# Kernel optimization log

Hardware: AMD Instinct MI355X
Metric: run time of the kernel (lower is better)

Reference implementation:

```python
import jax, jax.numpy as jnp
import numpy as np


def _maxpool2(x):
    # 2x2 max pool, stride 2, on NCHW
    b, c, h, w = x.shape
    return x.reshape(b, c, h // 2, 2, w // 2, 2).max(axis=(3, 5))


def _conv1x1(w, x):
    # w: [out_c, in_c], x: [B, in_c, H, W]
    return jnp.einsum('oc,bchw->bohw', w, x)


def setup_inputs() -> dict:
    key = jax.random.key(0)
    ks = jax.random.split(key, 5)
    B, C, H, W = 16, 64, 64, 64
    x = jax.random.normal(ks[0], (B, C, H, W), dtype=jnp.float32)
    # 1x1 conv weights (spectral-norm treated as already-normalized params)
    Wt = jax.random.normal(ks[1], (C // 8, C), dtype=jnp.float32) * 0.05
    Wp = jax.random.normal(ks[2], (C // 8, C), dtype=jnp.float32) * 0.05
    Wg = jax.random.normal(ks[3], (C // 2, C), dtype=jnp.float32) * 0.05
    Wo = jax.random.normal(ks[4], (C, C // 2), dtype=jnp.float32) * 0.05
    gamma = jnp.float32(0.5)  # nonzero so attention branch contributes
    return {"x": x, "Wt": Wt, "Wp": Wp, "Wg": Wg, "Wo": Wo, "gamma": gamma}


def reference(x, Wt, Wp, Wg, Wo, gamma):
    b, c, h, w = x.shape
    theta = _conv1x1(Wt, x).reshape(b, c // 8, h * w)            # [B, C/8, HW]
    phi = _maxpool2(_conv1x1(Wp, x)).reshape(b, c // 8, -1)      # [B, C/8, HW/4]
    g = _maxpool2(_conv1x1(Wg, x)).reshape(b, c // 2, -1)        # [B, C/2, HW/4]
    # scores: [B, HW, HW/4]; softmax over pooled (key) axis
    beta = jax.nn.softmax(jnp.einsum('bct,bcs->bts', theta, phi), axis=-1)
    o = jnp.einsum('bcs,bts->bct', g, beta).reshape(b, c // 2, h, w)
    o = _conv1x1(Wo, o)                                          # [B, C, H, W]
    return gamma * o + x
```

## Files before the change

### kernel.cpp

```cpp
#include <hip/hip_runtime.h>
#include <math.h>

#define NB   16
#define NC   64
#define HWs  4096
#define NPS  1024
#define LOG2E 1.44269504088896341f

static constexpr size_t PHI_OFF = (size_t)NB * HWs * 8;
static constexpr size_t GT_OFF  = PHI_OFF + (size_t)NB * NPS * 8;

typedef short s16x8 __attribute__((ext_vector_type(8)));
typedef float f32x4 __attribute__((ext_vector_type(4)));

#define LD8G(p) (*(const s16x8*)(p))
#define SB()    __builtin_amdgcn_sched_barrier(0)

__device__ inline unsigned short f2bf(float f) {
    unsigned int u = __float_as_uint(f);
    u += 0x7fffu + ((u >> 16) & 1u);
    return (unsigned short)(u >> 16);
}
__device__ inline unsigned int pk2(float a, float b) {
    unsigned int ua = __float_as_uint(a); ua += 0x7fffu + ((ua >> 16) & 1u);
    unsigned int ub = __float_as_uint(b); ub += 0x7fffu + ((ub >> 16) & 1u);
    return (ua >> 16) | (ub & 0xffff0000u);
}

__global__ __launch_bounds__(256) __attribute__((amdgpu_waves_per_eu(4, 4)))
void k_proj(
    const float* __restrict__ x, const float* __restrict__ Wt,
    const float* __restrict__ Wp, const float* __restrict__ Wg,
    unsigned short* __restrict__ ws)
{
    __shared__ float xs[64 * 128];

    unsigned short* theta = ws;
    unsigned short* phi   = ws + PHI_OFF;
    unsigned short* gT    = ws + GT_OFF;

    const int tid  = threadIdx.x;
    const int blk  = blockIdx.x;
    const int b    = blk >> 6;
    const int rp   = (blk >> 1) & 31;
    const int half = blk & 1;

    const float* xsrc = x + (size_t)b * NC * HWs + rp * 128;
#pragma unroll
    for (int i = 0; i < 8; ++i) {
        const int idx = i * 256 + tid;
        const int ci  = idx >> 5;
        const int f4  = idx & 31;
        float4 v = *(const float4*)(xsrc + (size_t)ci * HWs + f4 * 4);
        *(float4*)(xs + ci * 128 + f4 * 4) = v;
    }
    __syncthreads();

    const int h   = tid & 127;
    const int sub = __builtin_amdgcn_readfirstlane(tid >> 7);
    const int row = h & 1;
    const int col = h >> 1;
    const int px  = row * 64 + col;

    float a4[4], ag8[8];
#pragma unroll
    for (int j = 0; j < 4; ++j) a4[j] = 0.f;
#pragma unroll
    for (int j = 0; j < 8; ++j) ag8[j] = 0.f;

    const float* W8 = (half ? Wp : Wt) + sub * 4 * NC;
    const float* WG = Wg + (half * 16 + sub * 8) * NC;

#pragma unroll 4
    for (int ci = 0; ci < NC; ++ci) {
        const float xv = xs[ci * 128 + px];
#pragma unroll
        for (int j = 0; j < 4; ++j) a4[j] += W8[j * NC + ci] * xv;
#pragma unroll
        for (int j = 0; j < 8; ++j) ag8[j] += WG[j * NC + ci] * xv;
    }

    if (half == 0) {
        const int q = (2 * rp + row) * 64 + col;
        uint2 pkd;
        pkd.x = pk2(a4[0] * LOG2E, a4[1] * LOG2E);
        pkd.y = pk2(a4[2] * LOG2E, a4[3] * LOG2E);
        *(uint2*)(theta + ((size_t)b * HWs + q) * 8 + sub * 4) = pkd;
    } else {
#pragma unroll
        for (int j = 0; j < 4; ++j) {
            float v = a4[j];
            v = fmaxf(v, __shfl_xor(v, 1));
            v = fmaxf(v, __shfl_xor(v, 2));
            a4[j] = v;
        }
    }

#pragma unroll
    for (int j = 0; j < 8; ++j) {
        float v = ag8[j];
        v = fmaxf(v, __shfl_xor(v, 1));
        v = fmaxf(v, __shfl_xor(v, 2));
        ag8[j] = v;
    }

    if ((h & 3) == 0) {
        const int ps = rp * 32 + (h >> 2);
        if (half == 1) {
            uint2 pkd;
            pkd.x = pk2(a4[0], a4[1]);
            pkd.y = pk2(a4[2], a4[3]);
            *(uint2*)(phi + ((size_t)b * NPS + ps) * 8 + sub * 4) = pkd;
        }
#pragma unroll
        for (int j = 0; j < 8; ++j) {
            const int c = half * 16 + sub * 8 + j;
            gT[((size_t)b * 32 + c) * NPS + ps] = f2bf(ag8[j]);
        }
    }
}

__global__ __launch_bounds__(256) __attribute__((amdgpu_waves_per_eu(4, 4)))
void k_attn(
    const float* __restrict__ x, const float* __restrict__ Wo,
    const float* __restrict__ gamma_p, const unsigned short* __restrict__ ws,
    float* __restrict__ out)
{
    __shared__ __align__(16) unsigned char smem[18432];

    const int tid  = threadIdx.x;
    const int wave = __builtin_amdgcn_readfirstlane(tid >> 6);
    const int lane = tid & 63;
    const int quad = lane >> 4, lr = lane & 15;
    const int blk  = blockIdx.x;
    const int b    = blk >> 6;
    const int q0   = (blk & 63) * 64;

    const unsigned short* th = ws + (size_t)b * HWs * 8;
    const unsigned short* ph = ws + PHI_OFF + (size_t)b * NPS * 8;
    const unsigned short* gp = ws + GT_OFF + (size_t)b * 32 * NPS;
    unsigned short* Pw = (unsigned short*)smem + wave * 2304;

    const s16x8 zf = {0, 0, 0, 0, 0, 0, 0, 0};
    const f32x4 zc = {0.f, 0.f, 0.f, 0.f};

    const s16x8 thA = (quad == 0) ? LD8G(th + (size_t)(q0 + wave * 16 + lr) * 8) : zf;

    f32x4 O[2];
    f32x4 l4;
#pragma unroll
    for (int r = 0; r < 4; ++r) { O[0][r] = 0.f; O[1][r] = 0.f; l4[r] = 0.f; }

    const int voff_ph0 = (0 * 16 + lr) * 16;
    const int voff_ph1 = (1 * 16 + lr) * 16;
    const int voff_ph2 = (2 * 16 + lr) * 16;
    const int voff_ph3 = (3 * 16 + lr) * 16;
    const int voff_g00 = ((0 * 16 + lr) * NPS + 0 * 32 + quad * 8) * 2;
    const int voff_g01 = ((1 * 16 + lr) * NPS + 0 * 32 + quad * 8) * 2;
    const int voff_g10 = ((0 * 16 + lr) * NPS + 1 * 32 + quad * 8) * 2;
    const int voff_g11 = ((1 * 16 + lr) * NPS + 1 * 32 + quad * 8) * 2;

    s16x8 phB_e[4], phB_o[4];
    s16x8 Gf_e[2][2], Gf_o[2][2];

#define GL4(dst, off, base)                                                   \
    asm volatile("global_load_dwordx4 %0, %1, %2"                             \
                 : "=v"(dst) : "v"(off), "s"(base) : "memory")

#define LOADPH_A(dst, baseT)                                                  \
    GL4(dst[0], voff_ph0, baseT); GL4(dst[1], voff_ph1, baseT);               \
    GL4(dst[2], voff_ph2, baseT); GL4(dst[3], voff_ph3, baseT);

#define LOADG_A(dst, baseT)                                                   \
    GL4(dst[0][0], voff_g00, baseT); GL4(dst[0][1], voff_g01, baseT);         \
    GL4(dst[1][0], voff_g10, baseT); GL4(dst[1][1], voff_g11, baseT);

#define WAITVM(n) asm volatile("s_waitcnt vmcnt(" #n ")" ::: "memory")

#define QK(Sv, phB)                                                           \
    _Pragma("unroll")                                                         \
    for (int ss = 0; ss < 4; ++ss)                                            \
        Sv[ss] = __builtin_amdgcn_mfma_f32_16x16x32_bf16(thA, phB[ss], zc, 0, 0, 0);

#define EXPST(Sv, wbuf)                                                       \
    _Pragma("unroll")                                                         \
    for (int ss = 0; ss < 4; ++ss)                                            \
        _Pragma("unroll")                                                     \
        for (int r = 0; r < 4; ++r) {                                         \
            const float p = exp2f(Sv[ss][r]);                                 \
            l4[r] += p;                                                       \
            Pw[(wbuf) + (quad * 4 + r) * 72 + ss * 16 + lr] =                 \
                (unsigned short)(__float_as_uint(p) >> 16);                   \
        }

#define BODY(phCUR, GfPREV, GfCUR, phNXT, curT, rbuf, wbuf)                   \
    {                                                                         \
        const unsigned short* gbT  = gp + (size_t)(curT) * 64;                \
        const unsigned short* phT1 = ph + (size_t)((curT) + 1) * 512;         \
        LOADG_A(GfCUR, gbT);                                                  \
        LOADPH_A(phNXT, phT1);                                                \
        const s16x8 Pf0 = *(const s16x8*)(Pw + (rbuf) + lr * 72 + quad * 8);  \
        const s16x8 Pf1 = *(const s16x8*)(Pw + (rbuf) + lr * 72 + 32 + quad * 8); \
        WAITVM(8);                                                            \
        SB();                                                                 \
        f32x4 S[4];                                                           \
        QK(S, phCUR);                                                         \
        _Pragma("unroll")                                                     \
        for (int cs = 0; cs < 2; ++cs)                                        \
            O[cs] = __builtin_amdgcn_mfma_f32_16x16x32_bf16(Pf0, GfPREV[0][cs], O[cs], 0, 0, 0); \
        _Pragma("unroll")                                                     \
        for (int cs = 0; cs < 2; ++cs)                                        \
            O[cs] = __builtin_amdgcn_mfma_f32_16x16x32_bf16(Pf1, GfPREV[1][cs], O[cs], 0, 0, 0); \
        EXPST(S, wbuf);                                                       \
    }

    LOADPH_A(phB_e, ph);
    LOADG_A(Gf_e, gp);
    {
        const unsigned short* ph1 = ph + 512;
        LOADPH_A(phB_o, ph1);
    }
    WAITVM(8);
    SB();
    {
        f32x4 S[4];
        QK(S, phB_e);
        EXPST(S, 0);
    }

    for (int t = 1; t < 15; t += 2) {
        BODY(phB_o, Gf_e, Gf_o, phB_e, t,     0,    1152);
        BODY(phB_e, Gf_o, Gf_e, phB_o, t + 1, 1152, 0);
    }

    {
        const unsigned short* gb15 = gp + (size_t)15 * 64;
        LOADG_A(Gf_o, gb15);
        const s16x8 Pf0 = *(const s16x8*)(Pw + 0 + lr * 72 + quad * 8);
        const s16x8 Pf1 = *(const s16x8*)(Pw + 0 + lr * 72 + 32 + quad * 8);
        WAITVM(4);
        SB();
        f32x4 S[4];
        QK(S, phB_o);
#pragma unroll
        for (int cs = 0; cs < 2; ++cs)
            O[cs] = __builtin_amdgcn_mfma_f32_16x16x32_bf16(Pf0, Gf_e[0][cs], O[cs], 0, 0, 0);
#pragma unroll
        for (int cs = 0; cs < 2; ++cs)
            O[cs] = __builtin_amdgcn_mfma_f32_16x16x32_bf16(Pf1, Gf_e[1][cs], O[cs], 0, 0, 0);
        EXPST(S, 1152);
    }

    {
        WAITVM(0);
        SB();
        const s16x8 Pf0 = *(const s16x8*)(Pw + 1152 + lr * 72 + quad * 8);
        const s16x8 Pf1 = *(const s16x8*)(Pw + 1152 + lr * 72 + 32 + quad * 8);
#pragma unroll
        for (int cs = 0; cs < 2; ++cs)
            O[cs] = __builtin_amdgcn_mfma_f32_16x16x32_bf16(Pf0, Gf_o[0][cs], O[cs], 0, 0, 0);
#pragma unroll
        for (int cs = 0; cs < 2; ++cs)
            O[cs] = __builtin_amdgcn_mfma_f32_16x16x32_bf16(Pf1, Gf_o[1][cs], O[cs], 0, 0, 0);
    }

#pragma unroll
    for (int r = 0; r < 4; ++r) {
        float v = l4[r];
        v += __shfl_xor(v, 1);
        v += __shfl_xor(v, 2);
        v += __shfl_xor(v, 4);
        v += __shfl_xor(v, 8);
        l4[r] = 1.f / v;
    }

    __syncthreads();
    float* otile = (float*)smem;
#pragma unroll
    for (int cs = 0; cs < 2; ++cs) {
        f32x4 v;
#pragma unroll
        for (int r = 0; r < 4; ++r) v[r] = O[cs][r] * l4[r];
        *(f32x4*)(otile + (cs * 16 + lr) * 68 + wave * 16 + quad * 4) = v;
    }
    __syncthreads();

    const int qq = tid & 63;
    const int quarter = __builtin_amdgcn_readfirstlane(tid >> 6);
    float ov[32];
#pragma unroll
    for (int c = 0; c < 32; ++c) ov[c] = otile[c * 68 + qq];
    const float gam = gamma_p[0];
#pragma unroll
    for (int j = 0; j < 16; ++j) {
        const float* wrow = Wo + (size_t)(quarter * 16 + j) * 32;
        float a = 0.f;
#pragma unroll
        for (int c = 0; c < 32; ++c) a += wrow[c] * ov[c];
        const size_t ad = ((size_t)b * NC + quarter * 16 + j) * HWs + q0 + qq;
        out[ad] = gam * a + x[ad];
    }
}

extern "C" void kernel_launch(void* const* d_in, const int* in_sizes, int n_in,
                              void* d_out, int out_size, void* d_ws, size_t ws_size,
                              hipStream_t stream) {
    const float* x     = (const float*)d_in[0];
    const float* Wt    = (const float*)d_in[1];
    const float* Wp    = (const float*)d_in[2];
    const float* Wg    = (const float*)d_in[3];
    const float* Wo    = (const float*)d_in[4];
    const float* gamma = (const float*)d_in[5];
    float* out = (float*)d_out;
    unsigned short* ws = (unsigned short*)d_ws;

    k_proj<<<1024, 256, 0, stream>>>(x, Wt, Wp, Wg, ws);
    k_attn<<<1024, 256, 0, stream>>>(x, Wo, gamma, ws, out);
}
```

Before: 128.4 us.

## Stage G tiles cooperatively through swizzled LDS and stagger key-tile order per block

Previously each wave loaded its own four G fragments per key tile straight from global memory. Now the block loads each G tile once, cooperatively, with one 16-byte load per thread. The tile goes into a double-buffered, XOR-swizzled LDS staging area, and each wave then reads its fragments from LDS. Blocks also start at a different key tile (blk & 15) to spread L2/HBM traffic. This cuts redundant global loads by four but adds a __syncthreads per tile and more LDS, which may lower occupancy.

```diff
diff --git a/kernel.cpp b/kernel.cpp
--- a/kernel.cpp
+++ b/kernel.cpp
@@ -126,7 +126,7 @@
     const float* __restrict__ gamma_p, const unsigned short* __restrict__ ws,
     float* __restrict__ out)
 {
-    __shared__ __align__(16) unsigned char smem[18432];
+    __shared__ __align__(16) unsigned char smem[26624];
 
     const int tid  = threadIdx.x;
     const int wave = __builtin_amdgcn_readfirstlane(tid >> 6);
@@ -135,11 +135,18 @@
     const int blk  = blockIdx.x;
     const int b    = blk >> 6;
     const int q0   = (blk & 63) * 64;
+    const int stoff = blk & 15;
 
     const unsigned short* th = ws + (size_t)b * HWs * 8;
     const unsigned short* ph = ws + PHI_OFF + (size_t)b * NPS * 8;
     const unsigned short* gp = ws + GT_OFF + (size_t)b * 32 * NPS;
-    unsigned short* Pw = (unsigned short*)smem + wave * 2304;
+    unsigned short* Pw  = (unsigned short*)smem + wave * 2304;
+    unsigned short* stg = (unsigned short*)(smem + 18432);
+
+    const int sch   = tid >> 3;
+    const int spart = tid & 7;
+    const int swz   = spart ^ (sch & 7);
+    const int voff_gc = sch * (NPS * 2) + spart * 16;
 
     const s16x8 zf = {0, 0, 0, 0, 0, 0, 0, 0};
     const f32x4 zc = {0.f, 0.f, 0.f, 0.f};
@@ -155,13 +162,9 @@
     const int voff_ph1 = (1 * 16 + lr) * 16;
     const int voff_ph2 = (2 * 16 + lr) * 16;
     const int voff_ph3 = (3 * 16 + lr) * 16;
-    const int voff_g00 = ((0 * 16 + lr) * NPS + 0 * 32 + quad * 8) * 2;
-    const int voff_g01 = ((1 * 16 + lr) * NPS + 0 * 32 + quad * 8) * 2;
-    const int voff_g10 = ((0 * 16 + lr) * NPS + 1 * 32 + quad * 8) * 2;
-    const int voff_g11 = ((1 * 16 + lr) * NPS + 1 * 32 + quad * 8) * 2;
 
     s16x8 phB_e[4], phB_o[4];
-    s16x8 Gf_e[2][2], Gf_o[2][2];
+    s16x8 greg_e, greg_o;
 
 #define GL4(dst, off, base)                                                   \
     asm volatile("global_load_dwordx4 %0, %1, %2"                             \
@@ -170,10 +173,6 @@
 #define LOADPH_A(dst, baseT)                                                  \
     GL4(dst[0], voff_ph0, baseT); GL4(dst[1], voff_ph1, baseT);               \
     GL4(dst[2], voff_ph2, baseT); GL4(dst[3], voff_ph3, baseT);
-
-#define LOADG_A(dst, baseT)                                                   \
-    GL4(dst[0][0], voff_g00, baseT); GL4(dst[0][1], voff_g01, baseT);         \
-    GL4(dst[1][0], voff_g10, baseT); GL4(dst[1][1], voff_g11, baseT);
 
 #define WAITVM(n) asm volatile("s_waitcnt vmcnt(" #n ")" ::: "memory")
 
@@ -193,75 +192,78 @@
                 (unsigned short)(__float_as_uint(p) >> 16);                   \
         }
 
-#define BODY(phCUR, GfPREV, GfCUR, phNXT, curT, rbuf, wbuf)                   \
+#define BODY(phCUR, phNXT, gCUR, gNXT, curT, LAST)                            \
     {                                                                         \
-        const unsigned short* gbT  = gp + (size_t)(curT) * 64;                \
-        const unsigned short* phT1 = ph + (size_t)((curT) + 1) * 512;         \
-        LOADG_A(GfCUR, gbT);                                                  \
-        LOADPH_A(phNXT, phT1);                                                \
-        const s16x8 Pf0 = *(const s16x8*)(Pw + (rbuf) + lr * 72 + quad * 8);  \
-        const s16x8 Pf1 = *(const s16x8*)(Pw + (rbuf) + lr * 72 + 32 + quad * 8); \
-        WAITVM(8);                                                            \
+        WAITVM(4);              \
+        __syncthreads();                                                      \
+        *(s16x8*)(stg + ((curT) & 1) * 2048 + sch * 64 + swz * 8) = gCUR;     \
+        if (!(LAST)) {                                                        \
+            const int stn = ((curT) + 1 + stoff) & 15;                        \
+            GL4(gNXT, voff_gc, gp + (size_t)stn * 64);                        \
+            LOADPH_A(phNXT, ph + (size_t)stn * 512);                          \
+        }                                                                     \
+        const int pb = ((curT) - 1) & 1;                                      \
+        const s16x8 Pf0 = *(const s16x8*)(Pw + pb * 1152 + lr * 72 + quad * 8);      \
+        const s16x8 Pf1 = *(const s16x8*)(Pw + pb * 1152 + lr * 72 + 32 + quad * 8); \
+        s16x8 Gf[2][2];                                                       \
+        _Pragma("unroll")                                                     \
+        for (int kc = 0; kc < 2; ++kc)                                        \
+            _Pragma("unroll")                                                 \
+            for (int cs = 0; cs < 2; ++cs)                                    \
+                Gf[kc][cs] = *(const s16x8*)(stg + pb * 2048 +                \
+                    (cs * 16 + lr) * 64 + ((kc * 4 + quad) ^ (lr & 7)) * 8);  \
+        if (LAST) { WAITVM(0); } else { WAITVM(5); }       \
         SB();                                                                 \
         f32x4 S[4];                                                           \
         QK(S, phCUR);                                                         \
         _Pragma("unroll")                                                     \
         for (int cs = 0; cs < 2; ++cs)                                        \
-            O[cs] = __builtin_amdgcn_mfma_f32_16x16x32_bf16(Pf0, GfPREV[0][cs], O[cs], 0, 0, 0); \
+            O[cs] = __builtin_amdgcn_mfma_f32_16x16x32_bf16(Pf0, Gf[0][cs], O[cs], 0, 0, 0); \
         _Pragma("unroll")                                                     \
         for (int cs = 0; cs < 2; ++cs)                                        \
-            O[cs] = __builtin_amdgcn_mfma_f32_16x16x32_bf16(Pf1, GfPREV[1][cs], O[cs], 0, 0, 0); \
-        EXPST(S, wbuf);                                                       \
-    }
-
-    LOADPH_A(phB_e, ph);
-    LOADG_A(Gf_e, gp);
+            O[cs] = __builtin_amdgcn_mfma_f32_16x16x32_bf16(Pf1, Gf[1][cs], O[cs], 0, 0, 0); \
+        EXPST(S, ((curT) & 1) * 1152);                                        \
+    }
+
     {
-        const unsigned short* ph1 = ph + 512;
-        LOADPH_A(phB_o, ph1);
-    }
-    WAITVM(8);
-    SB();
-    {
+        const int st0 = stoff;
+        const int st1 = (stoff + 1) & 15;
+        GL4(greg_e, voff_gc, gp + (size_t)st0 * 64);
+        LOADPH_A(phB_e, ph + (size_t)st0 * 512);
+        WAITVM(4);
+        *(s16x8*)(stg + 0 * 2048 + sch * 64 + swz * 8) = greg_e;
+        GL4(greg_o, voff_gc, gp + (size_t)st1 * 64);
+        LOADPH_A(phB_o, ph + (size_t)st1 * 512);
+        WAITVM(5);
+        SB();
         f32x4 S[4];
         QK(S, phB_e);
         EXPST(S, 0);
     }
 
     for (int t = 1; t < 15; t += 2) {
-        BODY(phB_o, Gf_e, Gf_o, phB_e, t,     0,    1152);
-        BODY(phB_e, Gf_o, Gf_e, phB_o, t + 1, 1152, 0);
-    }
+        BODY(phB_o, phB_e, greg_o, greg_e, t,     0);
+        BODY(phB_e, phB_o, greg_e, greg_o, t + 1, 0);
+    }
+    BODY(phB_o, phB_e, greg_o, greg_e, 15, 1);
 
     {
-        const unsigned short* gb15 = gp + (size_t)15 * 64;
-        LOADG_A(Gf_o, gb15);
-        const s16x8 Pf0 = *(const s16x8*)(Pw + 0 + lr * 72 + quad * 8);
-        const s16x8 Pf1 = *(const s16x8*)(Pw + 0 + lr * 72 + 32 + quad * 8);
-        WAITVM(4);
-        SB();
-        f32x4 S[4];
-        QK(S, phB_o);
-#pragma unroll
-        for (int cs = 0; cs < 2; ++cs)
-            O[cs] = __builtin_amdgcn_mfma_f32_16x16x32_bf16(Pf0, Gf_e[0][cs], O[cs], 0, 0, 0);
-#pragma unroll
-        for (int cs = 0; cs < 2; ++cs)
-            O[cs] = __builtin_amdgcn_mfma_f32_16x16x32_bf16(Pf1, Gf_e[1][cs], O[cs], 0, 0, 0);
-        EXPST(S, 1152);
-    }
-
-    {
-        WAITVM(0);
-        SB();
+        __syncthreads();
         const s16x8 Pf0 = *(const s16x8*)(Pw + 1152 + lr * 72 + quad * 8);
         const s16x8 Pf1 = *(const s16x8*)(Pw + 1152 + lr * 72 + 32 + quad * 8);
+        s16x8 Gf[2][2];
+#pragma unroll
+        for (int kc = 0; kc < 2; ++kc)
+#pragma unroll
+            for (int cs = 0; cs < 2; ++cs)
+                Gf[kc][cs] = *(const s16x8*)(stg + 2048 +
+                    (cs * 16 + lr) * 64 + ((kc * 4 + quad) ^ (lr & 7)) * 8);
 #pragma unroll
         for (int cs = 0; cs < 2; ++cs)
-            O[cs] = __builtin_amdgcn_mfma_f32_16x16x32_bf16(Pf0, Gf_o[0][cs], O[cs], 0, 0, 0);
+            O[cs] = __builtin_amdgcn_mfma_f32_16x16x32_bf16(Pf0, Gf[0][cs], O[cs], 0, 0, 0);
 #pragma unroll
         for (int cs = 0; cs < 2; ++cs)
-            O[cs] = __builtin_amdgcn_mfma_f32_16x16x32_bf16(Pf1, Gf_o[1][cs], O[cs], 0, 0, 0);
+            O[cs] = __builtin_amdgcn_mfma_f32_16x16x32_bf16(Pf1, Gf[1][cs], O[cs], 0, 0, 0);
     }
 
 #pragma unroll
```

Result: faster. 114.2 us (-11.0%).
